# Kernel tuning notes

Measured on AMD Instinct MI355X. Metric: run time of the kernel, lower is better.

The kernel has to match this reference:

```python
import jax, jax.numpy as jnp
import numpy as np

H, D = 2, 64          # heads, hidden_dim per head
HD = H * D            # 128
N_NODES = 50000
N_EDGES = 800000
N_GRAPHS = 64
IN_CH, EDGE_DIM, N_CLASSES = 2, 1, 30


def _tconv(x, src, dst, Wq, bq, Wk, bk, Wv, bv, We, Ws, bs):
    """PyG TransformerConv (concat=True, root_weight=True, beta=False)."""
    n = x.shape[0]
    q = (x @ Wq + bq).reshape(n, H, D)
    k = (x @ Wk + bk).reshape(n, H, D)
    v = (x @ Wv + bv).reshape(n, H, D)
    # edge embedding (lin_edge has no bias in PyG)
    return _attend(q, k, v, x @ Ws + bs, src, dst, We, n)


def _attend(q, k, v, skip, src, dst, We_e, n):
    kj = k[src] + We_e            # [E,H,D]
    vj = v[src] + We_e
    logits = (q[dst] * kj).sum(-1) / jnp.sqrt(jnp.asarray(D, q.dtype))  # [E,H]
    m = jax.ops.segment_max(logits, dst, num_segments=n)
    m = jnp.where(jnp.isfinite(m), m, jnp.zeros_like(m))
    ex = jnp.exp(logits - m[dst])
    denom = jax.ops.segment_sum(ex, dst, num_segments=n)
    alpha = ex / (denom[dst] + 1e-16)                                   # segment softmax
    agg = jax.ops.segment_sum(alpha[..., None] * vj, dst, num_segments=n)
    return agg.reshape(n, HD) + skip


def _forward(x, edge_index, edge_attr, batch,
             l0_Wq, l0_bq, l0_Wk, l0_bk, l0_Wv, l0_bv, l0_We, l0_Ws, l0_bs,
             l1_Wq, l1_bq, l1_Wk, l1_bk, l1_Wv, l1_bv, l1_We, l1_Ws, l1_bs,
             cW1, cb1, cW2, cb2):
    src, dst = edge_index[0], edge_index[1]
    e0 = (edge_attr @ l0_We).reshape(-1, H, D)
    e1 = (edge_attr @ l1_We).reshape(-1, H, D)
    n = x.shape[0]

    h = _attend((x @ l0_Wq + l0_bq).reshape(n, H, D),
                (x @ l0_Wk + l0_bk).reshape(n, H, D),
                (x @ l0_Wv + l0_bv).reshape(n, H, D),
                x @ l0_Ws + l0_bs, src, dst, e0, n)
    h = jax.nn.relu(h)
    h = _attend((h @ l1_Wq + l1_bq).reshape(n, H, D),
                (h @ l1_Wk + l1_bk).reshape(n, H, D),
                (h @ l1_Wv + l1_bv).reshape(n, H, D),
                h @ l1_Ws + l1_bs, src, dst, e1, n)
    h = jax.nn.relu(h)

    # global_mean_pool over graphs
    sums = jax.ops.segment_sum(h, batch, num_segments=N_GRAPHS)
    cnt = jax.ops.segment_sum(jnp.ones((n,), h.dtype), batch, num_segments=N_GRAPHS)
    g = sums / jnp.maximum(cnt, 1.0)[:, None]                           # [G, 128]

    return jax.nn.relu(g @ cW1 + cb1) @ cW2 + cb2                       # [G, 30]


def setup_inputs() -> dict:
    key = jax.random.key(0)
    ks = jax.random.split(key, 40)
    it = iter(ks)

    def lin(k, fan_in, fan_out):
        s = 1.0 / np.sqrt(fan_in)
        return jax.random.uniform(k, (fan_in, fan_out), jnp.float32, -s, s)

    inp = {
        'x': jax.random.normal(next(it), (N_NODES, IN_CH), jnp.float32),
        'edge_index': jax.random.randint(next(it), (2, N_EDGES), 0, N_NODES),
        'edge_attr': jax.random.normal(next(it), (N_EDGES, EDGE_DIM), jnp.float32),
        'batch': jnp.sort(jax.random.randint(next(it), (N_NODES,), 0, N_GRAPHS)),
    }
    for li, cin in (('l0', IN_CH), ('l1', HD)):
        for nm in ('Wq', 'Wk', 'Wv'):
            inp[f'{li}_{nm}'] = lin(next(it), cin, HD)
            inp[f'{li}_{nm.replace("W", "b")}'] = jax.random.uniform(
                next(it), (HD,), jnp.float32, -1 / np.sqrt(cin), 1 / np.sqrt(cin))
        inp[f'{li}_We'] = lin(next(it), EDGE_DIM, HD)
        inp[f'{li}_Ws'] = lin(next(it), cin, HD)
        inp[f'{li}_bs'] = jax.random.uniform(next(it), (HD,), jnp.float32,
                                             -1 / np.sqrt(cin), 1 / np.sqrt(cin))
    inp['cW1'] = lin(next(it), HD, 128)
    inp['cb1'] = jax.random.uniform(next(it), (128,), jnp.float32, -1 / np.sqrt(HD), 1 / np.sqrt(HD))
    inp['cW2'] = lin(next(it), 128, N_CLASSES)
    inp['cb2'] = jax.random.uniform(next(it), (N_CLASSES,), jnp.float32, -1 / np.sqrt(128), 1 / np.sqrt(128))
    return inp


def reference(x, edge_index, edge_attr, batch,
              l0_Wq, l0_bq, l0_Wk, l0_bk, l0_Wv, l0_bv, l0_We, l0_Ws, l0_bs,
              l1_Wq, l1_bq, l1_Wk, l1_bk, l1_Wv, l1_bv, l1_We, l1_Ws, l1_bs,
              cW1, cb1, cW2, cb2):
    return _forward(x, edge_index, edge_attr, batch,
                    l0_Wq, l0_bq, l0_Wk, l0_bk, l0_Wv, l0_bv, l0_We, l0_Ws, l0_bs,
                    l1_Wq, l1_bq, l1_Wk, l1_bk, l1_Wv, l1_bv, l1_We, l1_Ws, l1_bs,
                    cW1, cb1, cW2, cb2)
```

## Files before the change

### kernel.cpp

```cpp
#include <hip/hip_runtime.h>
#include <hip/hip_fp16.h>
#include <cstdint>
#include <cstddef>

#define HD 128

typedef short bf16x8 __attribute__((ext_vector_type(8)));
typedef float f32x4 __attribute__((ext_vector_type(4)));

__device__ __forceinline__ unsigned short f2bf(float f) {
    unsigned int u = __float_as_uint(f);
    u += 0x7fff + ((u >> 16) & 1);
    return (unsigned short)(u >> 16);
}
__device__ __forceinline__ float bf2f(unsigned short h) {
    return __uint_as_float(((unsigned int)h) << 16);
}

template<int CTRL>
__device__ __forceinline__ float dpp_add(float x) {
    int y = __builtin_amdgcn_update_dpp(0, __float_as_int(x), CTRL, 0xF, 0xF, true);
    return x + __int_as_float(y);
}
__device__ __forceinline__ float half_reduce(float x) {
    x = dpp_add<0xB1>(x);
    x = dpp_add<0x4E>(x);
    x = dpp_add<0x124>(x);
    x = dpp_add<0x128>(x);
    x += __shfl_xor(x, 16, 64);
    return x;
}

__device__ __forceinline__ void pair_update_s(
    float& m, float& s, float2& acc,
    float lA, float lB,
    float vAx, float vAy, float vBx, float vBy)
{
    float nm = fmaxf(fmaxf(m, lA), lB);
    float sc = __expf(m - nm);
    float eA = __expf(lA - nm);
    float eB = __expf(lB - nm);
    s     = fmaf(s, sc, eA + eB);
    acc.x = fmaf(acc.x, sc, fmaf(eA, vAx, eB * vBx));
    acc.y = fmaf(acc.y, sc, fmaf(eA, vAy, eB * vBy));
    m = nm;
}
__device__ __forceinline__ void single_update_s(
    float& m, float& s, float2& acc,
    float lg, float vx, float vy)
{
    float nm = fmaxf(m, lg);
    float sc = __expf(m - nm);
    float ex = __expf(lg - nm);
    s     = fmaf(s, sc, ex);
    acc.x = fmaf(acc.x, sc, ex * vx);
    acc.y = fmaf(acc.y, sc, ex * vy);
    m = nm;
}

__global__ __launch_bounds__(256) void hist_kernel(
    const int* __restrict__ dst, int* __restrict__ cnt, int E)
{
    int e = blockIdx.x * 256 + threadIdx.x;
    if (e < E) atomicAdd(&cnt[dst[e]], 1);
}

__global__ __launch_bounds__(256) void scanA_kernel(
    const int* __restrict__ cnt, int* __restrict__ row_ptr,
    int* __restrict__ bsum, int n)
{
    __shared__ int sdata[256];
    int t = threadIdx.x;
    int base = blockIdx.x * 512 + 2 * t;
    int a = (base < n) ? cnt[base] : 0;
    int b = (base + 1 < n) ? cnt[base + 1] : 0;
    int local = a + b;
    sdata[t] = local;
    __syncthreads();
    #pragma unroll
    for (int off = 1; off < 256; off <<= 1) {
        int val = (t >= off) ? sdata[t - off] : 0;
        __syncthreads();
        sdata[t] += val;
        __syncthreads();
    }
    int excl = sdata[t] - local;
    if (base < n)     row_ptr[base] = excl;
    if (base + 1 < n) row_ptr[base + 1] = excl + a;
    if (t == 255) bsum[blockIdx.x] = sdata[255];
}

__global__ __launch_bounds__(256) void scanB_kernel(
    const int* __restrict__ bsum, int* __restrict__ boff, int B)
{
    __shared__ int sdata[256];
    int t = threadIdx.x;
    int local = (t < B) ? bsum[t] : 0;
    sdata[t] = local;
    __syncthreads();
    #pragma unroll
    for (int off = 1; off < 256; off <<= 1) {
        int val = (t >= off) ? sdata[t - off] : 0;
        __syncthreads();
        sdata[t] += val;
        __syncthreads();
    }
    if (t < B) boff[t] = sdata[t] - local;
}

__global__ __launch_bounds__(256) void scanC_kernel(
    int* __restrict__ row_ptr, int* __restrict__ cursor,
    const int* __restrict__ boff, int n, int E)
{
    int t = threadIdx.x;
    int base = blockIdx.x * 512 + 2 * t;
    int off = boff[blockIdx.x];
    if (base + 1 < n) {
        int2 v = *(int2*)&row_ptr[base];
        v.x += off; v.y += off;
        *(int2*)&row_ptr[base] = v;
        *(int2*)&cursor[base]  = v;
    } else if (base < n) {
        int v = row_ptr[base] + off;
        row_ptr[base] = v; cursor[base] = v;
    }
    if (blockIdx.x == 0 && t == 0) row_ptr[n] = E;
}

__global__ __launch_bounds__(256) void scatter_kernel(
    const int* __restrict__ dst, const int* __restrict__ src,
    const float* __restrict__ eattr, int* __restrict__ cursor,
    int2* __restrict__ epack, int E)
{
    int e = blockIdx.x * 256 + threadIdx.x;
    if (e < E) {
        int pos = atomicAdd(&cursor[dst[e]], 1);
        epack[pos] = make_int2(src[e], __float_as_int(eattr[e]));
    }
}

__global__ __launch_bounds__(256) void attn0_kernel(
    const float* __restrict__ x,
    const float* __restrict__ Wq, const float* __restrict__ bq,
    const float* __restrict__ Wk, const float* __restrict__ bk,
    const float* __restrict__ Wv, const float* __restrict__ bv,
    const float* __restrict__ We, const float* __restrict__ Ws,
    const float* __restrict__ bs,
    const int2* __restrict__ epack, const int* __restrict__ row_ptr,
    float* __restrict__ out, int n)
{
    int i = blockIdx.x * 4 + (threadIdx.x >> 6);
    if (i >= n) return;
    int l = threadIdx.x & 63;
    int j0 = 2 * l;

    float2 wk0 = *(const float2*)&Wk[j0];
    float2 wk1 = *(const float2*)&Wk[HD + j0];
    float2 wv0 = *(const float2*)&Wv[j0];
    float2 wv1 = *(const float2*)&Wv[HD + j0];
    float2 bk2 = *(const float2*)&bk[j0];
    float2 bv2 = *(const float2*)&bv[j0];
    float2 we  = *(const float2*)&We[j0];

    float x0 = x[2 * i], x1 = x[2 * i + 1];
    float2 wq0 = *(const float2*)&Wq[j0];
    float2 wq1 = *(const float2*)&Wq[HD + j0];
    float2 bq2 = *(const float2*)&bq[j0];
    float2 q;
    q.x = fmaf(x1, wq1.x, fmaf(x0, wq0.x, bq2.x));
    q.y = fmaf(x1, wq1.y, fmaf(x0, wq0.y, bq2.y));

    float c0 = half_reduce(fmaf(q.x, wk0.x, q.y * wk0.y)) * 0.125f;
    float c1 = half_reduce(fmaf(q.x, wk1.x, q.y * wk1.y)) * 0.125f;
    float cb = half_reduce(fmaf(q.x, bk2.x, q.y * bk2.y)) * 0.125f;
    float cw = half_reduce(fmaf(q.x, we.x,  q.y * we.y))  * 0.125f;

    int p0 = __builtin_amdgcn_readfirstlane(row_ptr[i]);
    int p1 = __builtin_amdgcn_readfirstlane(row_ptr[i + 1]);

    float m = -INFINITY, s = 0.f;
    float2 acc = make_float2(0.f, 0.f);

    float2 xs0 = {}, xs1 = {}, xs2 = {}, xs3 = {};
    float ea0 = 0.f, ea1 = 0.f, ea2 = 0.f, ea3 = 0.f;

#define LD0(t, idx) do { if ((idx) < p1) { int2 ep_ = epack[idx]; \
    ea##t = __int_as_float(ep_.y); xs##t = *(const float2*)&x[2 * ep_.x]; } } while (0)

#define LOGIT0(xs, ea) fmaf(ea, cw, fmaf(xs.y, c1, fmaf(xs.x, c0, cb)))
#define VREC(xs, ea, vx, vy) \
    float vx = fmaf(ea, we.x, fmaf(xs.y, wv1.x, fmaf(xs.x, wv0.x, bv2.x))); \
    float vy = fmaf(ea, we.y, fmaf(xs.y, wv1.y, fmaf(xs.x, wv0.y, bv2.y)));

    LD0(0, p0); LD0(1, p0 + 1); LD0(2, p0 + 2); LD0(3, p0 + 3);

    int p = p0;
    for (; p + 3 < p1; p += 4) {
        float2 c0v = xs0, c1v = xs1, c2v = xs2, c3v = xs3;
        float a0 = ea0, a1 = ea1, a2 = ea2, a3 = ea3;
        LD0(0, p + 4); LD0(1, p + 5); LD0(2, p + 6); LD0(3, p + 7);
        { VREC(c0v, a0, vAx, vAy) VREC(c1v, a1, vBx, vBy)
          pair_update_s(m, s, acc, LOGIT0(c0v, a0), LOGIT0(c1v, a1), vAx, vAy, vBx, vBy); }
        { VREC(c2v, a2, vAx, vAy) VREC(c3v, a3, vBx, vBy)
          pair_update_s(m, s, acc, LOGIT0(c2v, a2), LOGIT0(c3v, a3), vAx, vAy, vBx, vBy); }
    }
    int rem = p1 - p;
    if (rem >= 2) {
        VREC(xs0, ea0, vAx, vAy) VREC(xs1, ea1, vBx, vBy)
        pair_update_s(m, s, acc, LOGIT0(xs0, ea0), LOGIT0(xs1, ea1), vAx, vAy, vBx, vBy);
    }
    if (rem == 1) {
        VREC(xs0, ea0, vx, vy)
        single_update_s(m, s, acc, LOGIT0(xs0, ea0), vx, vy);
    } else if (rem == 3) {
        VREC(xs2, ea2, vx, vy)
        single_update_s(m, s, acc, LOGIT0(xs2, ea2), vx, vy);
    }

    float inv = 1.f / (s + 1e-16f);
    float2 ws0 = *(const float2*)&Ws[j0];
    float2 ws1 = *(const float2*)&Ws[HD + j0];
    float2 bs2 = *(const float2*)&bs[j0];
    float sk_x = fmaf(x1, ws1.x, fmaf(x0, ws0.x, bs2.x));
    float sk_y = fmaf(x1, ws1.y, fmaf(x0, ws0.y, bs2.y));
    float2 res;
    res.x = fmaxf(fmaf(acc.x, inv, sk_x), 0.f);
    res.y = fmaxf(fmaf(acc.y, inv, sk_y), 0.f);
    *(float2*)&out[(size_t)i * HD + j0] = res;
}

__global__ __launch_bounds__(256) void attn_kernel(
    const __half* __restrict__ qh, const __half* __restrict__ kvh,
    const __half* __restrict__ sh, const float* __restrict__ We,
    const int2* __restrict__ epack, const int* __restrict__ row_ptr,
    float* __restrict__ out, int n)
{
    int i = blockIdx.x * 4 + (threadIdx.x >> 6);
    if (i >= n) return;
    int l = threadIdx.x & 63;
    const int2* kv8 = (const int2*)kvh;
    const __half2* qh2 = (const __half2*)qh;
    const __half2* sh2 = (const __half2*)sh;
    float2 q  = __half22float2(qh2[(size_t)i * 64 + l]);
    float2 we = *(const float2*)&We[2 * l];
    int p0 = __builtin_amdgcn_readfirstlane(row_ptr[i]);
    int p1 = __builtin_amdgcn_readfirstlane(row_ptr[i + 1]);

    float m = -INFINITY, s = 0.f;
    float2 acc = make_float2(0.f, 0.f);

    int2 kv0 = {}, kv1 = {}, kv2 = {}, kv3 = {};
    float ea0 = 0.f, ea1 = 0.f, ea2 = 0.f, ea3 = 0.f;

#define LD1(t, idx) do { if ((idx) < p1) { int2 ep_ = epack[idx]; \
    ea##t = __int_as_float(ep_.y); kv##t = kv8[(size_t)ep_.x * 64 + l]; } } while (0)

#define KVX(raw, ea, kx, ky, vx, vy) \
    float2 kf_##kx = __half22float2(*(const __half2*)&raw.x); \
    float2 vf_##kx = __half22float2(*(const __half2*)&raw.y); \
    float kx = fmaf(ea, we.x, kf_##kx.x), ky = fmaf(ea, we.y, kf_##kx.y); \
    float vx = fmaf(ea, we.x, vf_##kx.x), vy = fmaf(ea, we.y, vf_##kx.y);

    LD1(0, p0); LD1(1, p0 + 1); LD1(2, p0 + 2); LD1(3, p0 + 3);

    int p = p0;
    for (; p + 3 < p1; p += 4) {
        int2 c0 = kv0, c1 = kv1, c2 = kv2, c3 = kv3;
        float a0 = ea0, a1 = ea1, a2 = ea2, a3 = ea3;
        LD1(0, p + 4); LD1(1, p + 5); LD1(2, p + 6); LD1(3, p + 7);
        {
            KVX(c0, a0, kAx, kAy, vAx, vAy)
            KVX(c1, a1, kBx, kBy, vBx, vBy)
            float lA = half_reduce(fmaf(q.x, kAx, q.y * kAy)) * 0.125f;
            float lB = half_reduce(fmaf(q.x, kBx, q.y * kBy)) * 0.125f;
            pair_update_s(m, s, acc, lA, lB, vAx, vAy, vBx, vBy);
        }
        {
            KVX(c2, a2, kAx, kAy, vAx, vAy)
            KVX(c3, a3, kBx, kBy, vBx, vBy)
            float lA = half_reduce(fmaf(q.x, kAx, q.y * kAy)) * 0.125f;
            float lB = half_reduce(fmaf(q.x, kBx, q.y * kBy)) * 0.125f;
            pair_update_s(m, s, acc, lA, lB, vAx, vAy, vBx, vBy);
        }
    }
    int rem = p1 - p;
    if (rem >= 2) {
        KVX(kv0, ea0, kAx, kAy, vAx, vAy)
        KVX(kv1, ea1, kBx, kBy, vBx, vBy)
        float lA = half_reduce(fmaf(q.x, kAx, q.y * kAy)) * 0.125f;
        float lB = half_reduce(fmaf(q.x, kBx, q.y * kBy)) * 0.125f;
        pair_update_s(m, s, acc, lA, lB, vAx, vAy, vBx, vBy);
    }
    if (rem == 1) {
        KVX(kv0, ea0, kx, ky, vx, vy)
        single_update_s(m, s, acc, half_reduce(fmaf(q.x, kx, q.y * ky)) * 0.125f, vx, vy);
    } else if (rem == 3) {
        KVX(kv2, ea2, kx, ky, vx, vy)
        single_update_s(m, s, acc, half_reduce(fmaf(q.x, kx, q.y * ky)) * 0.125f, vx, vy);
    }

    float inv = 1.f / (s + 1e-16f);
    float2 skp = __half22float2(sh2[(size_t)i * 64 + l]);
    float2 res;
    res.x = fmaxf(fmaf(acc.x, inv, skp.x), 0.f);
    res.y = fmaxf(fmaf(acc.y, inv, skp.y), 0.f);
    *(float2*)&out[(size_t)i * HD + 2 * l] = res;
}

__global__ __launch_bounds__(256) void pack_kernel(
    const float* __restrict__ Wq, const float* __restrict__ Wk,
    const float* __restrict__ Wv, const float* __restrict__ Ws,
    const float* __restrict__ bq, const float* __restrict__ bk,
    const float* __restrict__ bv, const float* __restrict__ bs,
    unsigned short* __restrict__ Wph, unsigned short* __restrict__ Wpl,
    float* __restrict__ bias_cat)
{
    int id = blockIdx.x * 256 + threadIdx.x;
    if (id < 65536) {
        int j = id & 7, lane = (id >> 3) & 63, ks = (id >> 9) & 3, gnt = id >> 11;
        int k = ks * 32 + (lane >> 4) * 8 + j;
        int ncol = gnt * 16 + (lane & 15);
        int mat = ncol >> 7, d = ncol & 127;
        const float* W = (mat == 0) ? Wq : (mat == 1) ? Wk : (mat == 2) ? Wv : Ws;
        float w = W[k * HD + d];
        unsigned short hi = f2bf(w);
        Wph[id] = hi;
        Wpl[id] = f2bf(w - bf2f(hi));
    }
    if (id < 512) {
        int mat = id >> 7, d = id & 127;
        const float* b = (mat == 0) ? bq : (mat == 1) ? bk : (mat == 2) ? bv : bs;
        bias_cat[id] = b[d];
    }
}

__global__ __launch_bounds__(256) void lin1_mfma(
    const float* __restrict__ A,
    const unsigned short* __restrict__ Wph, const unsigned short* __restrict__ Wpl,
    const float* __restrict__ bias_cat,
    __half* __restrict__ qh, __half* __restrict__ kvh, __half* __restrict__ sh,
    int n)
{
    __shared__ float As[128 * 128];
    int tid = threadIdx.x;
    int row0 = blockIdx.x * 128;
    int yb = blockIdx.y;

    #pragma unroll
    for (int it = 0; it < 16; ++it) {
        int idx = (it * 256 + tid) * 4;
        int r = idx >> 7, c = idx & 127;
        float4 av = make_float4(0.f, 0.f, 0.f, 0.f);
        if (row0 + r < n) av = *(const float4*)&A[(size_t)(row0 + r) * HD + c];
        int sl = (c >> 2) ^ (r & 7);
        *(float4*)&As[r * 128 + sl * 4] = av;
    }
    __syncthreads();

    int wave = tid >> 6, lane = tid & 63;
    int m = lane & 15, quad = lane >> 4;

    bf16x8 ah[2][4], al[2][4];
    #pragma unroll
    for (int sub = 0; sub < 2; ++sub) {
        int r = wave * 32 + sub * 16 + m;
        const float* base = &As[r * 128];
        int sw = r & 7;
        #pragma unroll
        for (int ks = 0; ks < 4; ++ks) {
            int i40 = (ks * 8 + quad * 2) ^ sw;
            int i41 = (ks * 8 + quad * 2 + 1) ^ sw;
            float4 x0 = *(const float4*)&base[i40 * 4];
            float4 x1 = *(const float4*)&base[i41 * 4];
            float v[8] = {x0.x, x0.y, x0.z, x0.w, x1.x, x1.y, x1.z, x1.w};
            #pragma unroll
            for (int j = 0; j < 8; ++j) {
                unsigned short hi = f2bf(v[j]);
                ah[sub][ks][j] = (short)hi;
                al[sub][ks][j] = (short)f2bf(v[j] - bf2f(hi));
            }
        }
    }
    __syncthreads();

    const bf16x8* PH = (const bf16x8*)Wph;
    const bf16x8* PL = (const bf16x8*)Wpl;
    __half2* qh2 = (__half2*)qh;
    __half2* sh2 = (__half2*)sh;
    __half*  kvS = (__half*)As;

    #define GNT_OF(nt) ((yb == 0) ? (((nt) < 8) ? (nt) : (nt) + 16) : (nt) + 8)

    bf16x8 bhA[4], blA[4], bhB[4], blB[4];
    {
        int g0 = GNT_OF(0);
        #pragma unroll
        for (int ks = 0; ks < 4; ++ks) {
            bhA[ks] = PH[(g0 * 4 + ks) * 64 + lane];
            blA[ks] = PL[(g0 * 4 + ks) * 64 + lane];
        }
    }

    for (int nt = 0; nt < 16; ++nt) {
        int gnt = GNT_OF(nt);
        if (nt + 1 < 16) {
            int g2 = GNT_OF(nt + 1);
            #pragma unroll
            for (int ks = 0; ks < 4; ++ks) {
                bhB[ks] = PH[(g2 * 4 + ks) * 64 + lane];
                blB[ks] = PL[(g2 * 4 + ks) * 64 + lane];
            }
        }
        f32x4 acc0 = {0.f, 0.f, 0.f, 0.f};
        f32x4 acc1 = {0.f, 0.f, 0.f, 0.f};
        #pragma unroll
        for (int ks = 0; ks < 4; ++ks) {
            acc0 = __builtin_amdgcn_mfma_f32_16x16x32_bf16(ah[0][ks], bhA[ks], acc0, 0, 0, 0);
            acc1 = __builtin_amdgcn_mfma_f32_16x16x32_bf16(ah[1][ks], bhA[ks], acc1, 0, 0, 0);
            acc0 = __builtin_amdgcn_mfma_f32_16x16x32_bf16(ah[0][ks], blA[ks], acc0, 0, 0, 0);
            acc1 = __builtin_amdgcn_mfma_f32_16x16x32_bf16(ah[1][ks], blA[ks], acc1, 0, 0, 0);
            acc0 = __builtin_amdgcn_mfma_f32_16x16x32_bf16(al[0][ks], bhA[ks], acc0, 0, 0, 0);
            acc1 = __builtin_amdgcn_mfma_f32_16x16x32_bf16(al[1][ks], bhA[ks], acc1, 0, 0, 0);
        }
        int ocol = gnt * 16 + m;
        int d = ocol & 127;
        float bias = bias_cat[ocol];
        if (yb == 0) {
            __half2* dst = (gnt < 8) ? qh2 : sh2;
            bool evenl = (m & 1) == 0;
            #pragma unroll
            for (int sub = 0; sub < 2; ++sub) {
                f32x4 acc = sub ? acc1 : acc0;
                #pragma unroll
                for (int reg = 0; reg < 4; ++reg) {
                    int orow = row0 + wave * 32 + sub * 16 + quad * 4 + reg;
                    float val = acc[reg] + bias;
                    float other = __shfl_xor(val, 1, 64);
                    if (orow < n && evenl)
                        dst[(size_t)orow * 64 + (d >> 1)] = __floats2half2_rn(val, other);
                }
            }
        } else {
            int slot = 4 * (d >> 1) + (d & 1) + ((gnt >= 16) ? 2 : 0);
            #pragma unroll
            for (int sub = 0; sub < 2; ++sub) {
                f32x4 acc = sub ? acc1 : acc0;
                #pragma unroll
                for (int reg = 0; reg < 4; ++reg) {
                    int row_l = wave * 32 + sub * 16 + quad * 4 + reg;
                    kvS[row_l * 256 + slot] = __float2half(acc[reg] + bias);
                }
            }
        }
        #pragma unroll
        for (int ks = 0; ks < 4; ++ks) { bhA[ks] = bhB[ks]; blA[ks] = blB[ks]; }
    }

    if (yb == 1) {
        __syncthreads();
        const float4* kvS4 = (const float4*)kvS;
        float4* kvh4 = (float4*)kvh;
        #pragma unroll
        for (int it = 0; it < 16; ++it) {
            int idx = it * 256 + tid;
            int row = idx >> 5, c4 = idx & 31;
            if (row0 + row < n)
                kvh4[(size_t)(row0 + row) * 32 + c4] = kvS4[row * 32 + c4];
        }
    }
    #undef GNT_OF
}

__global__ __launch_bounds__(128) void pool_kernel(
    const float* __restrict__ h, const int* __restrict__ batch,
    float* __restrict__ gsums, float* __restrict__ gcnt, int n)
{
    __shared__ int sb[64];
    int i0 = blockIdx.x * 64;
    int d = threadIdx.x;
    int iend = i0 + 64; if (iend > n) iend = n;
    int csize = iend - i0;
    if (d < csize) sb[d] = batch[i0 + d];
    __syncthreads();
    if (csize <= 0) return;
    float local = 0.f;
    int cur = sb[0];
    int runc = 0;
    for (int i = i0; i < iend; ++i) {
        int g = sb[i - i0];
        if (g != cur) {
            atomicAdd(&gsums[(size_t)cur * HD + d], local);
            if (d == 0) atomicAdd(&gcnt[cur], (float)runc);
            local = 0.f; runc = 0; cur = g;
        }
        local += h[(size_t)i * HD + d];
        runc++;
    }
    atomicAdd(&gsums[(size_t)cur * HD + d], local);
    if (d == 0) atomicAdd(&gcnt[cur], (float)runc);
}

__global__ __launch_bounds__(128) void cls_kernel(
    const float* __restrict__ gsums, const float* __restrict__ gcnt,
    const float* __restrict__ cW1, const float* __restrict__ cb1,
    const float* __restrict__ cW2, const float* __restrict__ cb2,
    float* __restrict__ out)
{
    __shared__ float g[128];
    __shared__ float t[128];
    int gi = blockIdx.x, j = threadIdx.x;
    float c = fmaxf(gcnt[gi], 1.0f);
    g[j] = gsums[(size_t)gi * HD + j] / c;
    __syncthreads();
    float a = cb1[j];
    for (int k = 0; k < 128; ++k) a = fmaf(g[k], cW1[k * 128 + j], a);
    t[j] = fmaxf(a, 0.f);
    __syncthreads();
    if (j < 30) {
        float a2 = cb2[j];
        for (int k = 0; k < 128; ++k) a2 = fmaf(t[k], cW2[k * 30 + j], a2);
        out[gi * 30 + j] = a2;
    }
}

extern "C" void kernel_launch(void* const* d_in, const int* in_sizes, int n_in,
                              void* d_out, int out_size, void* d_ws, size_t ws_size,
                              hipStream_t stream)
{
    const float* x     = (const float*)d_in[0];
    const int*   ei    = (const int*)d_in[1];
    const float* eattr = (const float*)d_in[2];
    const int*   batch = (const int*)d_in[3];
    const float* l0_Wq = (const float*)d_in[4];
    const float* l0_bq = (const float*)d_in[5];
    const float* l0_Wk = (const float*)d_in[6];
    const float* l0_bk = (const float*)d_in[7];
    const float* l0_Wv = (const float*)d_in[8];
    const float* l0_bv = (const float*)d_in[9];
    const float* l0_We = (const float*)d_in[10];
    const float* l0_Ws = (const float*)d_in[11];
    const float* l0_bs = (const float*)d_in[12];
    const float* l1_Wq = (const float*)d_in[13];
    const float* l1_bq = (const float*)d_in[14];
    const float* l1_Wk = (const float*)d_in[15];
    const float* l1_bk = (const float*)d_in[16];
    const float* l1_Wv = (const float*)d_in[17];
    const float* l1_bv = (const float*)d_in[18];
    const float* l1_We = (const float*)d_in[19];
    const float* l1_Ws = (const float*)d_in[20];
    const float* l1_bs = (const float*)d_in[21];
    const float* cW1   = (const float*)d_in[22];
    const float* cb1   = (const float*)d_in[23];
    const float* cW2   = (const float*)d_in[24];
    const float* cb2   = (const float*)d_in[25];

    int n = in_sizes[0] / 2;
    int E = in_sizes[2];
    int G = out_size / 30;
    int B = (n + 511) / 512;

    size_t nd = (size_t)n * HD;
    float* h      = (float*)d_ws;
    __half* qh    = (__half*)(h + nd);
    __half* sh    = qh + nd;
    __half* kvh   = sh + nd;
    float* bias_cat = (float*)(kvh + (size_t)n * 256);
    unsigned short* Wph = (unsigned short*)(bias_cat + 512);
    unsigned short* Wpl = Wph + 65536;
    int2* epack   = (int2*)(Wpl + 65536);
    int* cnt      = (int*)(epack + E);
    int* row_ptr  = cnt + n;
    int* cursor   = row_ptr + n + 2;
    int* bsum     = cursor + n;
    int* boff     = bsum + 256;
    float* gsums  = (float*)(boff + 256);
    float* gcnt   = gsums + (size_t)G * HD;

    const int* srcI = ei;
    const int* dstI = ei + E;

    hipMemsetAsync(cnt, 0, (size_t)n * sizeof(int), stream);
    hipMemsetAsync(gsums, 0, ((size_t)G * HD + G) * sizeof(float), stream);

    hist_kernel<<<(E + 255) / 256, 256, 0, stream>>>(dstI, cnt, E);
    scanA_kernel<<<B, 256, 0, stream>>>(cnt, row_ptr, bsum, n);
    scanB_kernel<<<1, 256, 0, stream>>>(bsum, boff, B);
    scanC_kernel<<<B, 256, 0, stream>>>(row_ptr, cursor, boff, n, E);
    scatter_kernel<<<(E + 255) / 256, 256, 0, stream>>>(dstI, srcI, eattr, cursor, epack, E);

    pack_kernel<<<256, 256, 0, stream>>>(l1_Wq, l1_Wk, l1_Wv, l1_Ws,
                                         l1_bq, l1_bk, l1_bv, l1_bs,
                                         Wph, Wpl, bias_cat);

    attn0_kernel<<<(n + 3) / 4, 256, 0, stream>>>(
        x, l0_Wq, l0_bq, l0_Wk, l0_bk, l0_Wv, l0_bv, l0_We, l0_Ws, l0_bs,
        epack, row_ptr, h, n);

    lin1_mfma<<<dim3((n + 127) / 128, 2), 256, 0, stream>>>(
        h, Wph, Wpl, bias_cat, qh, kvh, sh, n);
    attn_kernel<<<(n + 3) / 4, 256, 0, stream>>>(
        qh, kvh, sh, l1_We, epack, row_ptr, h, n);

    pool_kernel<<<(n + 63) / 64, 128, 0, stream>>>(h, batch, gsums, gcnt, n);
    cls_kernel<<<G, 128, 0, stream>>>(gsums, gcnt, cW1, cb1, cW2, cb2, (float*)d_out);
}
```

Before: 392.2 us.

## Factor layer-0 attention into per-node scalar softmax moments plus a dense expand

Layer-0 inputs are only 2-dimensional, so each head's logit is a bilinear form in the source features and the value projection is linear. The change precomputes 24 head coefficients in a tiny kernel. One thread per node then accumulates softmax-weighted moments (sum, x0, x1, edge attribute) per head, and a separate elementwise kernel expands these moments through Wv/bv/We and adds the skip term. This replaces a wave-per-node loop doing 128-wide vector math per edge with scalar per-thread work, at the cost of two extra launches and a small intermediate buffer.

```diff
diff --git a/kernel.cpp b/kernel.cpp
--- a/kernel.cpp
+++ b/kernel.cpp
@@ -28,6 +28,11 @@
     x = dpp_add<0x124>(x);
     x = dpp_add<0x128>(x);
     x += __shfl_xor(x, 16, 64);
+    return x;
+}
+__device__ __forceinline__ float wave_reduce(float x) {
+    x = half_reduce(x);
+    x += __shfl_xor(x, 32, 64);
     return x;
 }
 
@@ -139,94 +144,101 @@
     }
 }
 
-__global__ __launch_bounds__(256) void attn0_kernel(
-    const float* __restrict__ x,
+__global__ __launch_bounds__(128) void coef0_kernel(
     const float* __restrict__ Wq, const float* __restrict__ bq,
     const float* __restrict__ Wk, const float* __restrict__ bk,
+    const float* __restrict__ We, float* __restrict__ coef)
+{
+    int w = threadIdx.x >> 6, l = threadIdx.x & 63;
+    int j = w * 64 + l;
+    float q0 = Wq[j], q1 = Wq[HD + j], qb = bq[j];
+    float kv[4] = {Wk[j], Wk[HD + j], bk[j], We[j]};
+    #pragma unroll
+    for (int t = 0; t < 4; ++t) {
+        float m0 = wave_reduce(kv[t] * q0);
+        float m1 = wave_reduce(kv[t] * q1);
+        float m2 = wave_reduce(kv[t] * qb);
+        if (l == 0) {
+            coef[w * 12 + t * 3 + 0] = m0 * 0.125f;
+            coef[w * 12 + t * 3 + 1] = m1 * 0.125f;
+            coef[w * 12 + t * 3 + 2] = m2 * 0.125f;
+        }
+    }
+}
+
+__global__ __launch_bounds__(256) void attn0a_kernel(
+    const float* __restrict__ x, const float* __restrict__ coef,
+    const int2* __restrict__ epack, const int* __restrict__ row_ptr,
+    float4* __restrict__ S, int n)
+{
+    int i = blockIdx.x * 256 + threadIdx.x;
+    if (i >= n) return;
+    float C[24];
+    #pragma unroll
+    for (int t = 0; t < 24; ++t) C[t] = coef[t];
+    float x0 = x[2 * i], x1 = x[2 * i + 1];
+    float c0A = fmaf(x1, C[1],  fmaf(x0, C[0],  C[2]));
+    float c1A = fmaf(x1, C[4],  fmaf(x0, C[3],  C[5]));
+    float cbA = fmaf(x1, C[7],  fmaf(x0, C[6],  C[8]));
+    float cwA = fmaf(x1, C[10], fmaf(x0, C[9],  C[11]));
+    float c0B = fmaf(x1, C[13], fmaf(x0, C[12], C[14]));
+    float c1B = fmaf(x1, C[16], fmaf(x0, C[15], C[17]));
+    float cbB = fmaf(x1, C[19], fmaf(x0, C[18], C[20]));
+    float cwB = fmaf(x1, C[22], fmaf(x0, C[21], C[23]));
+
+    int p0 = row_ptr[i], p1 = row_ptr[i + 1];
+    float mA = -INFINITY, sA = 0.f, SxA = 0.f, SyA = 0.f, SeA = 0.f;
+    float mB = -INFINITY, sB = 0.f, SxB = 0.f, SyB = 0.f, SeB = 0.f;
+
+    int2 epn = (p0 < p1) ? epack[p0] : make_int2(0, 0);
+    for (int p = p0; p < p1; ++p) {
+        int2 ep = epn;
+        if (p + 1 < p1) epn = epack[p + 1];
+        float ea = __int_as_float(ep.y);
+        float2 xs = *(const float2*)&x[2 * ep.x];
+        float lgA = fmaf(ea, cwA, fmaf(xs.y, c1A, fmaf(xs.x, c0A, cbA)));
+        float lgB = fmaf(ea, cwB, fmaf(xs.y, c1B, fmaf(xs.x, c0B, cbB)));
+        {
+            float nm = fmaxf(mA, lgA);
+            float sc = __expf(mA - nm);
+            float ex = __expf(lgA - nm);
+            sA  = fmaf(sA,  sc, ex);
+            SxA = fmaf(SxA, sc, ex * xs.x);
+            SyA = fmaf(SyA, sc, ex * xs.y);
+            SeA = fmaf(SeA, sc, ex * ea);
+            mA = nm;
+        }
+        {
+            float nm = fmaxf(mB, lgB);
+            float sc = __expf(mB - nm);
+            float ex = __expf(lgB - nm);
+            sB  = fmaf(sB,  sc, ex);
+            SxB = fmaf(SxB, sc, ex * xs.x);
+            SyB = fmaf(SyB, sc, ex * xs.y);
+            SeB = fmaf(SeB, sc, ex * ea);
+            mB = nm;
+        }
+    }
+    S[(size_t)i * 2]     = make_float4(sA, SxA, SyA, SeA);
+    S[(size_t)i * 2 + 1] = make_float4(sB, SxB, SyB, SeB);
+}
+
+__global__ __launch_bounds__(256) void attn0b_kernel(
+    const float* __restrict__ x, const float4* __restrict__ S,
     const float* __restrict__ Wv, const float* __restrict__ bv,
-    const float* __restrict__ We, const float* __restrict__ Ws,
-    const float* __restrict__ bs,
-    const int2* __restrict__ epack, const int* __restrict__ row_ptr,
+    const float* __restrict__ We,
+    const float* __restrict__ Ws, const float* __restrict__ bs,
     float* __restrict__ out, int n)
 {
-    int i = blockIdx.x * 4 + (threadIdx.x >> 6);
-    if (i >= n) return;
-    int l = threadIdx.x & 63;
-    int j0 = 2 * l;
-
-    float2 wk0 = *(const float2*)&Wk[j0];
-    float2 wk1 = *(const float2*)&Wk[HD + j0];
-    float2 wv0 = *(const float2*)&Wv[j0];
-    float2 wv1 = *(const float2*)&Wv[HD + j0];
-    float2 bk2 = *(const float2*)&bk[j0];
-    float2 bv2 = *(const float2*)&bv[j0];
-    float2 we  = *(const float2*)&We[j0];
-
+    int gid = blockIdx.x * 256 + threadIdx.x;
+    if (gid >= n * HD) return;
+    int i = gid >> 7, j = gid & 127, h = j >> 6;
+    float4 Sv = S[(size_t)i * 2 + h];
     float x0 = x[2 * i], x1 = x[2 * i + 1];
-    float2 wq0 = *(const float2*)&Wq[j0];
-    float2 wq1 = *(const float2*)&Wq[HD + j0];
-    float2 bq2 = *(const float2*)&bq[j0];
-    float2 q;
-    q.x = fmaf(x1, wq1.x, fmaf(x0, wq0.x, bq2.x));
-    q.y = fmaf(x1, wq1.y, fmaf(x0, wq0.y, bq2.y));
-
-    float c0 = half_reduce(fmaf(q.x, wk0.x, q.y * wk0.y)) * 0.125f;
-    float c1 = half_reduce(fmaf(q.x, wk1.x, q.y * wk1.y)) * 0.125f;
-    float cb = half_reduce(fmaf(q.x, bk2.x, q.y * bk2.y)) * 0.125f;
-    float cw = half_reduce(fmaf(q.x, we.x,  q.y * we.y))  * 0.125f;
-
-    int p0 = __builtin_amdgcn_readfirstlane(row_ptr[i]);
-    int p1 = __builtin_amdgcn_readfirstlane(row_ptr[i + 1]);
-
-    float m = -INFINITY, s = 0.f;
-    float2 acc = make_float2(0.f, 0.f);
-
-    float2 xs0 = {}, xs1 = {}, xs2 = {}, xs3 = {};
-    float ea0 = 0.f, ea1 = 0.f, ea2 = 0.f, ea3 = 0.f;
-
-#define LD0(t, idx) do { if ((idx) < p1) { int2 ep_ = epack[idx]; \
-    ea##t = __int_as_float(ep_.y); xs##t = *(const float2*)&x[2 * ep_.x]; } } while (0)
-
-#define LOGIT0(xs, ea) fmaf(ea, cw, fmaf(xs.y, c1, fmaf(xs.x, c0, cb)))
-#define VREC(xs, ea, vx, vy) \
-    float vx = fmaf(ea, we.x, fmaf(xs.y, wv1.x, fmaf(xs.x, wv0.x, bv2.x))); \
-    float vy = fmaf(ea, we.y, fmaf(xs.y, wv1.y, fmaf(xs.x, wv0.y, bv2.y)));
-
-    LD0(0, p0); LD0(1, p0 + 1); LD0(2, p0 + 2); LD0(3, p0 + 3);
-
-    int p = p0;
-    for (; p + 3 < p1; p += 4) {
-        float2 c0v = xs0, c1v = xs1, c2v = xs2, c3v = xs3;
-        float a0 = ea0, a1 = ea1, a2 = ea2, a3 = ea3;
-        LD0(0, p + 4); LD0(1, p + 5); LD0(2, p + 6); LD0(3, p + 7);
-        { VREC(c0v, a0, vAx, vAy) VREC(c1v, a1, vBx, vBy)
-          pair_update_s(m, s, acc, LOGIT0(c0v, a0), LOGIT0(c1v, a1), vAx, vAy, vBx, vBy); }
-        { VREC(c2v, a2, vAx, vAy) VREC(c3v, a3, vBx, vBy)
-          pair_update_s(m, s, acc, LOGIT0(c2v, a2), LOGIT0(c3v, a3), vAx, vAy, vBx, vBy); }
-    }
-    int rem = p1 - p;
-    if (rem >= 2) {
-        VREC(xs0, ea0, vAx, vAy) VREC(xs1, ea1, vBx, vBy)
-        pair_update_s(m, s, acc, LOGIT0(xs0, ea0), LOGIT0(xs1, ea1), vAx, vAy, vBx, vBy);
-    }
-    if (rem == 1) {
-        VREC(xs0, ea0, vx, vy)
-        single_update_s(m, s, acc, LOGIT0(xs0, ea0), vx, vy);
-    } else if (rem == 3) {
-        VREC(xs2, ea2, vx, vy)
-        single_update_s(m, s, acc, LOGIT0(xs2, ea2), vx, vy);
-    }
-
-    float inv = 1.f / (s + 1e-16f);
-    float2 ws0 = *(const float2*)&Ws[j0];
-    float2 ws1 = *(const float2*)&Ws[HD + j0];
-    float2 bs2 = *(const float2*)&bs[j0];
-    float sk_x = fmaf(x1, ws1.x, fmaf(x0, ws0.x, bs2.x));
-    float sk_y = fmaf(x1, ws1.y, fmaf(x0, ws0.y, bs2.y));
-    float2 res;
-    res.x = fmaxf(fmaf(acc.x, inv, sk_x), 0.f);
-    res.y = fmaxf(fmaf(acc.y, inv, sk_y), 0.f);
-    *(float2*)&out[(size_t)i * HD + j0] = res;
+    float num = fmaf(Wv[j], Sv.y, fmaf(Wv[HD + j], Sv.z,
+                fmaf(bv[j], Sv.x, We[j] * Sv.w)));
+    float sk = fmaf(x1, Ws[HD + j], fmaf(x0, Ws[j], bs[j]));
+    out[gid] = fmaxf(num / (Sv.x + 1e-16f) + sk, 0.f);
 }
 
 __global__ __launch_bounds__(256) void attn_kernel(
@@ -567,7 +579,9 @@
     float* bias_cat = (float*)(kvh + (size_t)n * 256);
     unsigned short* Wph = (unsigned short*)(bias_cat + 512);
     unsigned short* Wpl = Wph + 65536;
-    int2* epack   = (int2*)(Wpl + 65536);
+    float* coef   = (float*)(Wpl + 65536);
+    float4* S0    = (float4*)(coef + 32);
+    int2* epack   = (int2*)(S0 + (size_t)n * 2);
     int* cnt      = (int*)(epack + E);
     int* row_ptr  = cnt + n;
     int* cursor   = row_ptr + n + 2;
@@ -591,10 +605,12 @@
     pack_kernel<<<256, 256, 0, stream>>>(l1_Wq, l1_Wk, l1_Wv, l1_Ws,
                                          l1_bq, l1_bk, l1_bv, l1_bs,
                                          Wph, Wpl, bias_cat);
-
-    attn0_kernel<<<(n + 3) / 4, 256, 0, stream>>>(
-        x, l0_Wq, l0_bq, l0_Wk, l0_bk, l0_Wv, l0_bv, l0_We, l0_Ws, l0_bs,
-        epack, row_ptr, h, n);
+    coef0_kernel<<<1, 128, 0, stream>>>(l0_Wq, l0_bq, l0_Wk, l0_bk, l0_We, coef);
+
+    attn0a_kernel<<<(n + 255) / 256, 256, 0, stream>>>(
+        x, coef, epack, row_ptr, S0, n);
+    attn0b_kernel<<<(n * HD + 255) / 256, 256, 0, stream>>>(
+        x, S0, l0_Wv, l0_bv, l0_We, l0_Ws, l0_bs, h, n);
 
     lin1_mfma<<<dim3((n + 127) / 128, 2), 256, 0, stream>>>(
         h, Wph, Wpl, bias_cat, qh, kvh, sh, n);
```

After: 374.2 us. 1.05x faster.
